# Optimization experiments

Measured on AMD Instinct MI355X. Metric: run time of the kernel, lower is better.

Reference implementation:

```python
import jax, jax.numpy as jnp
import numpy as np

B, S, D = 8, 4096, 1024
DIL = 1


def _kaiming_fan_out(key, shape, fan_out):
    std = np.sqrt(2.0 / fan_out)
    return jax.random.normal(key, shape, dtype=jnp.float32) * std


def setup_inputs() -> dict:
    key = jax.random.key(0)
    ks = jax.random.split(key, 7)
    x = jax.random.normal(ks[0], (B, S, D), dtype=jnp.float32)
    # depthwise conv weights, torch Conv1d shape [out_ch, in_ch/groups, k] = [D, 1, k]
    # kaiming fan_out for conv: fan_out = out_channels/groups * k = k
    w3 = _kaiming_fan_out(ks[1], (D, 1, 3), 3)
    w5 = _kaiming_fan_out(ks[2], (D, 1, 5), 5)
    w7 = _kaiming_fan_out(ks[3], (D, 1, 7), 7)
    # scale_gate initialized to zeros in the module
    w_gate = jnp.zeros((3, D), dtype=jnp.float32)
    # linear kaiming fan_out: fan_out = out_features
    w_up = _kaiming_fan_out(ks[4], (2 * D, D), 2 * D)
    w_down = _kaiming_fan_out(ks[5], (D, D), D)
    return {"x": x, "w_up": w_up, "w_down": w_down, "w_gate": w_gate,
            "w3": w3, "w5": w5, "w7": w7}


def _dconv(v, w, dilation):
    # v: [B, S, D]; w: [D, 1, k] depthwise causal conv
    k = w.shape[-1]
    pad = (k - 1) * dilation
    h = jnp.transpose(v, (0, 2, 1))               # [B, D, S]
    h = jnp.pad(h, ((0, 0), (0, 0), (pad, 0)))    # causal left pad
    out = jax.lax.conv_general_dilated(
        h, w, window_strides=(1,), padding='VALID',
        rhs_dilation=(dilation,), feature_group_count=v.shape[-1],
        dimension_numbers=('NCH', 'OIH', 'NCH'))
    return jnp.transpose(out, (0, 2, 1))          # [B, S, D]


def reference(x, w_up, w_down, w_gate, w3, w5, w7):
    gv = jnp.einsum('bsd,ed->bse', x, w_up)       # [B, S, 2D]
    gate, val = jnp.split(gv, 2, axis=-1)
    gate = jax.nn.sigmoid(gate)
    c_fine = _dconv(val, w3, DIL)
    c_medium = _dconv(val, w5, DIL)
    c_coarse = _dconv(val, w7, DIL)
    scale_w = jax.nn.softmax(jnp.einsum('bsd,ed->bse', x, w_gate), axis=-1)  # [B, S, 3]
    fused = (scale_w[..., 0:1] * c_fine
             + scale_w[..., 1:2] * c_medium
             + scale_w[..., 2:3] * c_coarse)
    return jnp.einsum('bsd,ed->bse', fused * gate, w_down)
```

## Files before the change

kernel.cpp:

```cpp
#include <hip/hip_runtime.h>
#include <hip/hip_bf16.h>


#define MB 8
#define SS 4096
#define DD 1024
#define MM (MB * SS)
#define KD 1024

typedef __attribute__((ext_vector_type(8))) short short8;
typedef __attribute__((ext_vector_type(4))) float f32x4;

static __device__ __forceinline__ unsigned short f2bf(float f) {
    union { float f; unsigned u; } a; a.f = f;
    unsigned u = a.u;
    unsigned r = (u + 0x7FFFu + ((u >> 16) & 1u)) >> 16;
    return (unsigned short)r;
}
static __device__ __forceinline__ float bf2f(unsigned short b) {
    union { unsigned u; float f; } a; a.u = ((unsigned)b) << 16;
    return a.f;
}

__global__ void prep_misc(const float* __restrict__ w_up, const float* __restrict__ w_down,
                          const float* __restrict__ w3, const float* __restrict__ w5,
                          const float* __restrict__ w7,
                          ushort4* __restrict__ wub, ushort4* __restrict__ wdb,
                          float* __restrict__ wt) {
    const int n1 = 2048 * 1024 / 4, n2 = 1024 * 1024 / 4;
    int i = blockIdx.x * 256 + threadIdx.x;
    if (i < n1) {
        float4 v = ((const float4*)w_up)[i];
        ushort4 o; o.x = f2bf(v.x); o.y = f2bf(v.y); o.z = f2bf(v.z); o.w = f2bf(v.w);
        wub[i] = o;
    } else if (i < n1 + n2) {
        int j = i - n1;
        float4 v = ((const float4*)w_down)[j];
        ushort4 o; o.x = f2bf(v.x); o.y = f2bf(v.y); o.z = f2bf(v.z); o.w = f2bf(v.w);
        wdb[j] = o;
    } else if (i < n1 + n2 + DD) {
        int d = i - n1 - n2;
        #pragma unroll
        for (int j = 0; j < 3; j++) wt[j * DD + d] = w3[d * 3 + j];
        #pragma unroll
        for (int j = 0; j < 5; j++) wt[(3 + j) * DD + d] = w5[d * 5 + j];
        #pragma unroll
        for (int j = 0; j < 7; j++) wt[(8 + j) * DD + d] = w7[d * 7 + j];
    }
}

__global__ void scale_cvt(const float* __restrict__ x, const float* __restrict__ wg,
                          unsigned short* __restrict__ xb, float* __restrict__ sw, int M) {
    int gw = (int)((blockIdx.x * (size_t)blockDim.x + threadIdx.x) >> 6);
    int lane = threadIdx.x & 63;
    if (gw >= M) return;
    const float* xr = x + (size_t)gw * DD + lane * 16;
    float4 xv[4];
    #pragma unroll
    for (int q = 0; q < 4; q++) xv[q] = ((const float4*)xr)[q];

    float s0 = 0.f, s1 = 0.f, s2 = 0.f;
    #pragma unroll
    for (int q = 0; q < 4; q++) {
        float4 w0 = ((const float4*)(wg + lane * 16))[q];
        float4 w1 = ((const float4*)(wg + DD + lane * 16))[q];
        float4 w2 = ((const float4*)(wg + 2 * DD + lane * 16))[q];
        s0 += xv[q].x*w0.x + xv[q].y*w0.y + xv[q].z*w0.z + xv[q].w*w0.w;
        s1 += xv[q].x*w1.x + xv[q].y*w1.y + xv[q].z*w1.z + xv[q].w*w1.w;
        s2 += xv[q].x*w2.x + xv[q].y*w2.y + xv[q].z*w2.z + xv[q].w*w2.w;
    }

    short8 ob[2];
    #pragma unroll
    for (int q = 0; q < 4; q++) {
        ob[q >> 1][(q & 1) * 4 + 0] = (short)f2bf(xv[q].x);
        ob[q >> 1][(q & 1) * 4 + 1] = (short)f2bf(xv[q].y);
        ob[q >> 1][(q & 1) * 4 + 2] = (short)f2bf(xv[q].z);
        ob[q >> 1][(q & 1) * 4 + 3] = (short)f2bf(xv[q].w);
    }
    *(short8*)(xb + (size_t)gw * DD + lane * 16) = ob[0];
    *(short8*)(xb + (size_t)gw * DD + lane * 16 + 8) = ob[1];

    #pragma unroll
    for (int off = 32; off >= 1; off >>= 1) {
        s0 += __shfl_xor(s0, off);
        s1 += __shfl_xor(s1, off);
        s2 += __shfl_xor(s2, off);
    }
    if (lane == 0) {
        float mx = fmaxf(s0, fmaxf(s1, s2));
        float e0 = expf(s0 - mx), e1 = expf(s1 - mx), e2 = expf(s2 - mx);
        float inv = 1.f / (e0 + e1 + e2);
        sw[(size_t)gw * 3 + 0] = e0 * inv;
        sw[(size_t)gw * 3 + 1] = e1 * inv;
        sw[(size_t)gw * 3 + 2] = e2 * inv;
    }
}

template <int EPI, int NBN>
__global__ __launch_bounds__(1024, 4) void gemm16(
    const unsigned short* __restrict__ A,
    const unsigned short* __restrict__ W,
    unsigned short* __restrict__ og,
    unsigned short* __restrict__ ov,
    float* __restrict__ of)
{
    __shared__ __align__(16) char lds[131072];
    const int tid = threadIdx.x;
    const int wid = tid >> 6, lane = tid & 63;
    const int l15 = lane & 15, l4 = lane >> 4;
    const int wr = wid >> 2, wc = wid & 3;

    const int flat = blockIdx.x + gridDim.x * blockIdx.y;
    const int k8 = flat & 7, j = flat >> 3;
    const int bn = j % NBN;
    const int bm = j / NBN + k8 * 16;

    const unsigned short* Ablk = A + (size_t)bm * 256 * KD;
    const unsigned short* Wblk = W + (size_t)bn * 256 * KD;

    const int r0 = tid >> 2;
    const int cch8 = (((tid & 3) ^ ((r0 >> 1) & 3)) << 3);
    const int dst0 = tid * 16;

    const int swz = ((l15 >> 1) & 3) << 4;
    const int aoff0 = (wr * 64 + l15) * 64 + ((l4 * 16) ^ swz);
    const int boff0 = (wc * 64 + l15) * 64 + ((l4 * 16) ^ swz);

    f32x4 acc[4][4];
    #pragma unroll
    for (int m = 0; m < 4; m++)
        #pragma unroll
        for (int n = 0; n < 4; n++) acc[m][n] = (f32x4)0.f;

#define LDSA(r) (lds + (r) * 16384)
#define LDSB(r) (lds + 65536 + (r) * 16384)
#define STAGE1(gp, lb) __builtin_amdgcn_global_load_lds( \
        (const __attribute__((address_space(1))) void*)((gp) + (size_t)r0 * KD + cch8), \
        (__attribute__((address_space(3))) void*)((lb) + dst0), 16, 0, 0)

    STAGE1(Ablk +  0, LDSA(0)); STAGE1(Wblk +  0, LDSB(0));
    STAGE1(Ablk + 32, LDSA(1)); STAGE1(Wblk + 32, LDSB(1));
    STAGE1(Ablk + 64, LDSA(2)); STAGE1(Wblk + 64, LDSB(2));
    asm volatile("s_waitcnt vmcnt(4)" ::: "memory");
    __builtin_amdgcn_s_barrier();

#define PHASE(q, soff) do { \
    const char* ar = LDSA(q); const char* br = LDSB(q); \
    short8 af0 = *(const short8*)(ar + aoff0); \
    short8 af1 = *(const short8*)(ar + aoff0 + 1024); \
    short8 af2 = *(const short8*)(ar + aoff0 + 2048); \
    short8 af3 = *(const short8*)(ar + aoff0 + 3072); \
    short8 bf0 = *(const short8*)(br + boff0); \
    short8 bf1 = *(const short8*)(br + boff0 + 1024); \
    short8 bf2 = *(const short8*)(br + boff0 + 2048); \
    short8 bf3 = *(const short8*)(br + boff0 + 3072); \
    STAGE1(Ablk + (soff), LDSA(((q) + 3) & 3)); \
    STAGE1(Wblk + (soff), LDSB(((q) + 3) & 3)); \
    __builtin_amdgcn_s_setprio(1); \
    acc[0][0] = __builtin_amdgcn_mfma_f32_16x16x32_bf16(af0, bf0, acc[0][0], 0, 0, 0); \
    acc[0][1] = __builtin_amdgcn_mfma_f32_16x16x32_bf16(af0, bf1, acc[0][1], 0, 0, 0); \
    acc[0][2] = __builtin_amdgcn_mfma_f32_16x16x32_bf16(af0, bf2, acc[0][2], 0, 0, 0); \
    acc[0][3] = __builtin_amdgcn_mfma_f32_16x16x32_bf16(af0, bf3, acc[0][3], 0, 0, 0); \
    acc[1][0] = __builtin_amdgcn_mfma_f32_16x16x32_bf16(af1, bf0, acc[1][0], 0, 0, 0); \
    acc[1][1] = __builtin_amdgcn_mfma_f32_16x16x32_bf16(af1, bf1, acc[1][1], 0, 0, 0); \
    acc[1][2] = __builtin_amdgcn_mfma_f32_16x16x32_bf16(af1, bf2, acc[1][2], 0, 0, 0); \
    acc[1][3] = __builtin_amdgcn_mfma_f32_16x16x32_bf16(af1, bf3, acc[1][3], 0, 0, 0); \
    acc[2][0] = __builtin_amdgcn_mfma_f32_16x16x32_bf16(af2, bf0, acc[2][0], 0, 0, 0); \
    acc[2][1] = __builtin_amdgcn_mfma_f32_16x16x32_bf16(af2, bf1, acc[2][1], 0, 0, 0); \
    acc[2][2] = __builtin_amdgcn_mfma_f32_16x16x32_bf16(af2, bf2, acc[2][2], 0, 0, 0); \
    acc[2][3] = __builtin_amdgcn_mfma_f32_16x16x32_bf16(af2, bf3, acc[2][3], 0, 0, 0); \
    acc[3][0] = __builtin_amdgcn_mfma_f32_16x16x32_bf16(af3, bf0, acc[3][0], 0, 0, 0); \
    acc[3][1] = __builtin_amdgcn_mfma_f32_16x16x32_bf16(af3, bf1, acc[3][1], 0, 0, 0); \
    acc[3][2] = __builtin_amdgcn_mfma_f32_16x16x32_bf16(af3, bf2, acc[3][2], 0, 0, 0); \
    acc[3][3] = __builtin_amdgcn_mfma_f32_16x16x32_bf16(af3, bf3, acc[3][3], 0, 0, 0); \
    __builtin_amdgcn_s_setprio(0); \
    asm volatile("s_waitcnt vmcnt(4)" ::: "memory"); \
    __builtin_amdgcn_s_barrier(); \
  } while (0)

    #pragma unroll 1
    for (int it = 0; it < 8; ++it) {
        const int p0 = it * 4;
        const int g0 = (p0 + 3 < 31 ? p0 + 3 : 31) * 32;
        const int g1 = (p0 + 4 < 31 ? p0 + 4 : 31) * 32;
        const int g2 = (p0 + 5 < 31 ? p0 + 5 : 31) * 32;
        const int g3 = (p0 + 6 < 31 ? p0 + 6 : 31) * 32;
        PHASE(0, g0);
        PHASE(1, g1);
        PHASE(2, g2);
        PHASE(3, g3);
    }
    asm volatile("s_waitcnt vmcnt(0)" ::: "memory");

    const int grow0 = bm * 256 + wr * 64;
    const int gcol0 = bn * 256 + wc * 64;
    if (EPI == 0) {
        #pragma unroll
        for (int m = 0; m < 4; m++) {
            #pragma unroll
            for (int n = 0; n < 4; n++) {
                int gcol = gcol0 + n * 16 + l15;
                bool isgate = gcol < 1024;
                unsigned short* dst = isgate ? og : ov;
                int cc = isgate ? gcol : gcol - 1024;
                #pragma unroll
                for (int r = 0; r < 4; r++) {
                    int grow = grow0 + m * 16 + l4 * 4 + r;
                    float v = acc[m][n][r];
                    float o = isgate ? (1.f / (1.f + __expf(-v))) : v;
                    dst[(size_t)grow * 1024 + cc] = f2bf(o);
                }
            }
        }
    } else {
        #pragma unroll
        for (int m = 0; m < 4; m++) {
            #pragma unroll
            for (int n = 0; n < 4; n++) {
                int gcol = gcol0 + n * 16 + l15;
                #pragma unroll
                for (int r = 0; r < 4; r++) {
                    int grow = grow0 + m * 16 + l4 * 4 + r;
                    of[(size_t)grow * 1024 + gcol] = acc[m][n][r];
                }
            }
        }
    }
#undef PHASE
#undef STAGE1
#undef LDSA
#undef LDSB
}

__global__ __launch_bounds__(256) void conv_mix(
    const unsigned short* __restrict__ val,
    unsigned short* __restrict__ ga,
    const float* __restrict__ sw,
    const float* __restrict__ wt)
{
    const int tid = threadIdx.x;
    const int dg = tid & 63, sr = tid >> 6;
    const int half = blockIdx.x & 1;
    const size_t mgrp = (size_t)(blockIdx.x >> 1);
    const size_t m = mgrp * 4 + sr;
    const int s = (int)(m & (SS - 1));
    const int d0 = half * 512 + dg * 8;

    const float* w3t = wt;
    const float* w5t = wt + 3 * DD;
    const float* w7t = wt + 8 * DD;

    float c3[8], c5[8], c7[8];
    #pragma unroll
    for (int i = 0; i < 8; i++) { c3[i] = 0.f; c5[i] = 0.f; c7[i] = 0.f; }

    #pragma unroll
    for (int j = 0; j < 7; j++) {
        int soff = s - 6 + j;
        float v[8];
        if (soff >= 0) {
            short8 r = *(const short8*)(val + (m - 6 + j) * (size_t)DD + d0);
            #pragma unroll
            for (int i = 0; i < 8; i++) v[i] = bf2f((unsigned short)r[i]);
        } else {
            #pragma unroll
            for (int i = 0; i < 8; i++) v[i] = 0.f;
        }
        {
            const float4* p = (const float4*)(w7t + (size_t)j * DD + d0);
            float4 wa = p[0], wb = p[1];
            c7[0] += v[0]*wa.x; c7[1] += v[1]*wa.y; c7[2] += v[2]*wa.z; c7[3] += v[3]*wa.w;
            c7[4] += v[4]*wb.x; c7[5] += v[5]*wb.y; c7[6] += v[6]*wb.z; c7[7] += v[7]*wb.w;
        }
        if (j >= 2) {
            const float4* p = (const float4*)(w5t + (size_t)(j - 2) * DD + d0);
            float4 wa = p[0], wb = p[1];
            c5[0] += v[0]*wa.x; c5[1] += v[1]*wa.y; c5[2] += v[2]*wa.z; c5[3] += v[3]*wa.w;
            c5[4] += v[4]*wb.x; c5[5] += v[5]*wb.y; c5[6] += v[6]*wb.z; c5[7] += v[7]*wb.w;
        }
        if (j >= 4) {
            const float4* p = (const float4*)(w3t + (size_t)(j - 4) * DD + d0);
            float4 wa = p[0], wb = p[1];
            c3[0] += v[0]*wa.x; c3[1] += v[1]*wa.y; c3[2] += v[2]*wa.z; c3[3] += v[3]*wa.w;
            c3[4] += v[4]*wb.x; c3[5] += v[5]*wb.y; c3[6] += v[6]*wb.z; c3[7] += v[7]*wb.w;
        }
    }

    float s0 = sw[m * 3 + 0], s1 = sw[m * 3 + 1], s2 = sw[m * 3 + 2];
    short8 g = *(const short8*)(ga + m * (size_t)DD + d0);
    short8 o;
    #pragma unroll
    for (int i = 0; i < 8; i++) {
        float fused = s0 * c3[i] + s1 * c5[i] + s2 * c7[i];
        o[i] = (short)f2bf(fused * bf2f((unsigned short)g[i]));
    }
    *(short8*)(ga + m * (size_t)DD + d0) = o;
}

extern "C" void kernel_launch(void* const* d_in, const int* in_sizes, int n_in,
                              void* d_out, int out_size, void* d_ws, size_t ws_size,
                              hipStream_t stream) {
    const float* x      = (const float*)d_in[0];
    const float* w_up   = (const float*)d_in[1];
    const float* w_down = (const float*)d_in[2];
    const float* w_gate = (const float*)d_in[3];
    const float* w3     = (const float*)d_in[4];
    const float* w5     = (const float*)d_in[5];
    const float* w7     = (const float*)d_in[6];
    float* out = (float*)d_out;

    char* ws = (char*)d_ws;
    const size_t NX = (size_t)MM * DD;
    unsigned short* xb   = (unsigned short*)ws;
    unsigned short* wub  = (unsigned short*)(ws + NX * 2);
    unsigned short* wdb  = (unsigned short*)(ws + NX * 2 + 4194304);
    unsigned short* gate = (unsigned short*)(ws + NX * 2 + 6291456);
    unsigned short* valb = (unsigned short*)(ws + NX * 2 + 6291456 + NX * 2);
    float*          sw   = (float*)(ws + NX * 2 + 6291456 + NX * 4);
    float*          wt   = (float*)(ws + NX * 2 + 6291456 + NX * 4 + 393216);

    prep_misc<<<(2048*1024/4 + 1024*1024/4 + DD + 255) / 256, 256, 0, stream>>>(
        w_up, w_down, w3, w5, w7, (ushort4*)wub, (ushort4*)wdb, wt);
    scale_cvt<<<MM / 4, 256, 0, stream>>>(x, w_gate, xb, sw, MM);
    gemm16<0, 8><<<dim3(MM / 256, 2048 / 256), 1024, 0, stream>>>(xb, wub, gate, valb, nullptr);
    conv_mix<<<MM / 4 * 2, 256, 0, stream>>>(valb, gate, sw, wt);
    gemm16<1, 4><<<dim3(MM / 256, 1024 / 256), 1024, 0, stream>>>(gate, wdb, nullptr, nullptr, out);
    (void)in_sizes; (void)n_in; (void)out_size; (void)ws_size;
}
```

Measured before the change: 435.4 us.

## Tile depthwise conv over 32-row chunks with LDS staging and register sliding window

Rewrites conv_mix so each block stages 38 rows of val (32 outputs plus a 6-row halo) in shared memory. Each thread keeps all 15 conv weights for its 8 channels in registers and slides a 7-row window down 16 rows. Previously every output row re-read 7 input rows and reloaded the weights from global memory, so this removes most redundant global and L2 traffic. The cost is heavy register pressure (120 floats of weights plus a 56-float window) and about 76KB of LDS per block, which may reduce occupancy.

Measured after the change: 352.4 us. 19.1% less time.

```diff
diff --git a/kernel.cpp b/kernel.cpp
--- a/kernel.cpp
+++ b/kernel.cpp
@@ -7,6 +7,7 @@
 #define DD 1024
 #define MM (MB * SS)
 #define KD 1024
+#define CR 32
 
 typedef __attribute__((ext_vector_type(8))) short short8;
 typedef __attribute__((ext_vector_type(4))) float f32x4;
@@ -239,63 +240,72 @@
     const float* __restrict__ sw,
     const float* __restrict__ wt)
 {
+    __shared__ unsigned short vlds[(CR + 6) * DD];
     const int tid = threadIdx.x;
-    const int dg = tid & 63, sr = tid >> 6;
-    const int half = blockIdx.x & 1;
-    const size_t mgrp = (size_t)(blockIdx.x >> 1);
-    const size_t m = mgrp * 4 + sr;
-    const int s = (int)(m & (SS - 1));
-    const int d0 = half * 512 + dg * 8;
-
-    const float* w3t = wt;
-    const float* w5t = wt + 3 * DD;
-    const float* w7t = wt + 8 * DD;
-
-    float c3[8], c5[8], c7[8];
-    #pragma unroll
-    for (int i = 0; i < 8; i++) { c3[i] = 0.f; c5[i] = 0.f; c7[i] = 0.f; }
-
-    #pragma unroll
-    for (int j = 0; j < 7; j++) {
-        int soff = s - 6 + j;
-        float v[8];
-        if (soff >= 0) {
-            short8 r = *(const short8*)(val + (m - 6 + j) * (size_t)DD + d0);
-            #pragma unroll
-            for (int i = 0; i < 8; i++) v[i] = bf2f((unsigned short)r[i]);
-        } else {
-            #pragma unroll
-            for (int i = 0; i < 8; i++) v[i] = 0.f;
-        }
+    const size_t r0 = (size_t)blockIdx.x * CR;
+    const int sbase = (int)(r0 & (SS - 1));
+
+    for (int idx = tid; idx < (CR + 6) * (DD / 8); idx += 256) {
+        const int row = idx >> 7;
+        const int chs = idx & 127;
+        short8 v;
+        if (sbase - 6 + row >= 0)
+            v = *(const short8*)(val + (r0 - 6 + row) * (size_t)DD + chs * 8);
+        else {
+            #pragma unroll
+            for (int i = 0; i < 8; i++) v[i] = 0;
+        }
+        *(short8*)(&vlds[row * DD + chs * 8]) = v;
+    }
+    __syncthreads();
+
+    const int ch = tid & 127;
+    const int rg = tid >> 7;
+    const int d0 = ch * 8;
+    const int k0 = rg * 16;
+
+    float fw[15][8];
+    #pragma unroll
+    for (int j = 0; j < 15; j++) {
+        float4 a = *(const float4*)(wt + j * DD + d0);
+        float4 b = *(const float4*)(wt + j * DD + d0 + 4);
+        fw[j][0] = a.x; fw[j][1] = a.y; fw[j][2] = a.z; fw[j][3] = a.w;
+        fw[j][4] = b.x; fw[j][5] = b.y; fw[j][6] = b.z; fw[j][7] = b.w;
+    }
+
+    float fwin[7][8];
+    #pragma unroll
+    for (int jj = 0; jj < 6; jj++) {
+        short8 v = *(const short8*)(&vlds[(k0 + jj) * DD + d0]);
+        #pragma unroll
+        for (int i = 0; i < 8; i++) fwin[jj][i] = bf2f((unsigned short)v[i]);
+    }
+
+    #pragma unroll
+    for (int k = 0; k < 16; k++) {
         {
-            const float4* p = (const float4*)(w7t + (size_t)j * DD + d0);
-            float4 wa = p[0], wb = p[1];
-            c7[0] += v[0]*wa.x; c7[1] += v[1]*wa.y; c7[2] += v[2]*wa.z; c7[3] += v[3]*wa.w;
-            c7[4] += v[4]*wb.x; c7[5] += v[5]*wb.y; c7[6] += v[6]*wb.z; c7[7] += v[7]*wb.w;
-        }
-        if (j >= 2) {
-            const float4* p = (const float4*)(w5t + (size_t)(j - 2) * DD + d0);
-            float4 wa = p[0], wb = p[1];
-            c5[0] += v[0]*wa.x; c5[1] += v[1]*wa.y; c5[2] += v[2]*wa.z; c5[3] += v[3]*wa.w;
-            c5[4] += v[4]*wb.x; c5[5] += v[5]*wb.y; c5[6] += v[6]*wb.z; c5[7] += v[7]*wb.w;
-        }
-        if (j >= 4) {
-            const float4* p = (const float4*)(w3t + (size_t)(j - 4) * DD + d0);
-            float4 wa = p[0], wb = p[1];
-            c3[0] += v[0]*wa.x; c3[1] += v[1]*wa.y; c3[2] += v[2]*wa.z; c3[3] += v[3]*wa.w;
-            c3[4] += v[4]*wb.x; c3[5] += v[5]*wb.y; c3[6] += v[6]*wb.z; c3[7] += v[7]*wb.w;
-        }
-    }
-
-    float s0 = sw[m * 3 + 0], s1 = sw[m * 3 + 1], s2 = sw[m * 3 + 2];
-    short8 g = *(const short8*)(ga + m * (size_t)DD + d0);
-    short8 o;
-    #pragma unroll
-    for (int i = 0; i < 8; i++) {
-        float fused = s0 * c3[i] + s1 * c5[i] + s2 * c7[i];
-        o[i] = (short)f2bf(fused * bf2f((unsigned short)g[i]));
-    }
-    *(short8*)(ga + m * (size_t)DD + d0) = o;
+            short8 v = *(const short8*)(&vlds[(k0 + k + 6) * DD + d0]);
+            #pragma unroll
+            for (int i = 0; i < 8; i++) fwin[(k + 6) % 7][i] = bf2f((unsigned short)v[i]);
+        }
+        const size_t m = r0 + k0 + k;
+        const float s0 = sw[m * 3 + 0], s1 = sw[m * 3 + 1], s2 = sw[m * 3 + 2];
+        short8 g = *(const short8*)(ga + m * DD + d0);
+        short8 o;
+        #pragma unroll
+        for (int i = 0; i < 8; i++) {
+            float c7v = 0.f, c5v = 0.f, c3v = 0.f;
+            #pragma unroll
+            for (int t = 0; t < 7; t++) c7v += fwin[(k + t) % 7][i] * fw[8 + t][i];
+            #pragma unroll
+            for (int t = 0; t < 5; t++) c5v += fwin[(k + t + 2) % 7][i] * fw[3 + t][i];
+            #pragma unroll
+            for (int t = 0; t < 3; t++) c3v += fwin[(k + t + 4) % 7][i] * fw[t][i];
+            float fused = s0 * c3v + s1 * c5v + s2 * c7v;
+            o[i] = (short)f2bf(fused * bf2f((unsigned short)g[i]));
+        }
+        *(short8*)(ga + m * DD + d0) = o;
+    }
 }
 
 extern "C" void kernel_launch(void* const* d_in, const int* in_sizes, int n_in,
@@ -324,7 +334,7 @@
         w_up, w_down, w3, w5, w7, (ushort4*)wub, (ushort4*)wdb, wt);
     scale_cvt<<<MM / 4, 256, 0, stream>>>(x, w_gate, xb, sw, MM);
     gemm16<0, 8><<<dim3(MM / 256, 2048 / 256), 1024, 0, stream>>>(xb, wub, gate, valb, nullptr);
-    conv_mix<<<MM / 4 * 2, 256, 0, stream>>>(valb, gate, sw, wt);
+    conv_mix<<<MM / CR, 256, 0, stream>>>(valb, gate, sw, wt);
     gemm16<1, 4><<<dim3(MM / 256, 1024 / 256), 1024, 0, stream>>>(gate, wdb, nullptr, nullptr, out);
     (void)in_sizes; (void)n_in; (void)out_size; (void)ws_size;
 }
```
